# Performance work log

Hardware: AMD Instinct MI355X
Metric: run time of the kernel (lower is better)

## Reference

```python
import jax, jax.numpy as jnp
import numpy as np

NUM_GROUPS = 32
EPS = 1e-6


def group_norm(x, scale, bias):
    # x: [b, c, l]
    b, c, l = x.shape
    xg = x.reshape(b, NUM_GROUPS, (c // NUM_GROUPS) * l)
    mean = jnp.mean(xg, axis=2, keepdims=True)
    var = jnp.var(xg, axis=2, keepdims=True)
    xn = ((xg - mean) * jax.lax.rsqrt(var + EPS)).reshape(b, c, l)
    return xn * scale[None, :, None] + bias[None, :, None]


def conv1x1(x, w, b):
    # pointwise conv: w [out_c, in_c], x [b, in_c, l]
    return jnp.einsum('oc,bcl->bol', w, x) + b[None, :, None]


def setup_inputs() -> dict:
    key = jax.random.key(0)
    ks = jax.random.split(key, 11)
    b, c, l = 4, 512, 4096
    s = 1.0 / np.sqrt(c)
    return {
        'x': jax.random.normal(ks[0], (b, c, l), jnp.float32),
        'gn_scale': jnp.ones((c,), jnp.float32),
        'gn_bias': jnp.zeros((c,), jnp.float32),
        'wq': jax.random.normal(ks[1], (c, c), jnp.float32) * s,
        'bq': jnp.zeros((c,), jnp.float32),
        'wk': jax.random.normal(ks[2], (c, c), jnp.float32) * s,
        'bk': jnp.zeros((c,), jnp.float32),
        'wv': jax.random.normal(ks[3], (c, c), jnp.float32) * s,
        'bv': jnp.zeros((c,), jnp.float32),
        'wp': jax.random.normal(ks[4], (c, c), jnp.float32) * s,
        'bp': jnp.zeros((c,), jnp.float32),
    }


def reference(x, gn_scale, gn_bias, wq, bq, wk, bk, wv, bv, wp, bp):
    h_ = group_norm(x, gn_scale, gn_bias)
    q = conv1x1(h_, wq, bq)  # [b, c, l]
    k = conv1x1(h_, wk, bk)
    v = conv1x1(h_, wv, bv)
    c = q.shape[1]
    # scores w[b,i,j] = sum_c q[b,c,i] k[b,c,j] * c^-0.5, softmax over j
    w = jnp.einsum('bci,bcj->bij', q, k) * (c ** -0.5)
    w = jax.nn.softmax(w, axis=2)
    # out[b,c,i] = sum_j w[b,i,j] v[b,c,j]
    h_ = jnp.einsum('bij,bcj->bci', w, v)
    h_ = conv1x1(h_, wp, bp)
    return x + h_
```

## Files before the change

kernel.cpp:

```cpp
#include <hip/hip_runtime.h>
#include <math.h>

#define BB 4
#define CC 512
#define LL 4096
#define NG 32
#define CPG 16
#define EPSV 1e-6f

typedef short s16x8 __attribute__((ext_vector_type(8)));
typedef __bf16 bf8v __attribute__((ext_vector_type(8)));
typedef float f32x4 __attribute__((ext_vector_type(4)));
typedef float f32x16 __attribute__((ext_vector_type(16)));
typedef int i32x4 __attribute__((ext_vector_type(4)));
typedef int i32x8 __attribute__((ext_vector_type(8)));
typedef unsigned short u16;
typedef unsigned char u8;

typedef const __attribute__((address_space(1))) void g1_void;
typedef __attribute__((address_space(3))) void l3_void;

#define ASM_SBAR() asm volatile("s_barrier" ::: "memory")
#define ASM_WAITV(N) asm volatile("s_waitcnt vmcnt(" #N ")" ::: "memory")

static __device__ __forceinline__ float bf2f(u16 h) {
    unsigned int u = ((unsigned int)h) << 16;
    union { unsigned int u; float f; } c; c.u = u; return c.f;
}
static __device__ __forceinline__ u16 f2bf(float f) {
    union { float f; unsigned int u; } c; c.f = f;
    unsigned int lsb = (c.u >> 16) & 1u;
    c.u += 0x7fffu + lsb;
    return (u16)(c.u >> 16);
}
static __device__ __forceinline__ u8 f2fp8(float f) {
    int v = __builtin_amdgcn_cvt_pk_fp8_f32(f, f, 0, false);
    return (u8)(v & 0xff);
}
static __device__ __forceinline__ bf8v ld_bf8(const u16* p) {
    return *reinterpret_cast<const bf8v*>(p);
}
static __device__ __forceinline__ i32x8 ld32(const u8* plo, const u8* phi) {
    i32x4 lo = *reinterpret_cast<const i32x4*>(plo);
    i32x4 hi = *reinterpret_cast<const i32x4*>(phi);
    return __builtin_shufflevector(lo, hi, 0, 1, 2, 3, 4, 5, 6, 7);
}
#define MFMA_SC(a, b, c) \
    __builtin_amdgcn_mfma_scale_f32_32x32x64_f8f6f4(a, b, c, 0, 0, 0, 0x7f, 0, 0x7f)

static __device__ __forceinline__ void gload16(const u16* g, u16* l) {
    __builtin_amdgcn_global_load_lds((g1_void*)g, (l3_void*)l, 16, 0, 0);
}
static __device__ __forceinline__ void gload16b(const u8* g, u8* l) {
    __builtin_amdgcn_global_load_lds((g1_void*)g, (l3_void*)l, 16, 0, 0);
}

__global__ __launch_bounds__(256) void wconv_kernel(const float* __restrict__ w0,
                                                    const float* __restrict__ w1,
                                                    const float* __restrict__ w2,
                                                    const float* __restrict__ w3,
                                                    u16* __restrict__ wbf) {
    int i = blockIdx.x * 256 + threadIdx.x;
    int wsel = blockIdx.y;
    const float* src = (wsel == 0) ? w0 : (wsel == 1) ? w1 : (wsel == 2) ? w2 : w3;
    float4 v = reinterpret_cast<const float4*>(src)[i];
    ushort4 o;
    o.x = f2bf(v.x); o.y = f2bf(v.y); o.z = f2bf(v.z); o.w = f2bf(v.w);
    reinterpret_cast<ushort4*>(wbf + (size_t)wsel * CC * CC)[i] = o;
}

__global__ __launch_bounds__(256) void biascat_kernel(const float* __restrict__ bq,
                                                      const float* __restrict__ bk,
                                                      const float* __restrict__ bv,
                                                      float* __restrict__ bcat,
                                                      float* __restrict__ rowsum) {
    int i = blockIdx.x * 256 + threadIdx.x;
    if (i < 3 * CC) {
        float v = (i < CC) ? bq[i] : (i < 2 * CC ? bk[i - CC] : bv[i - 2 * CC]);
        bcat[i] = v;
    }
    if (i < BB * LL) rowsum[i] = 0.f;
}

__global__ __launch_bounds__(256) void gn_stats_kernel(const float* __restrict__ x,
                                                       float2* __restrict__ stats) {
    int g = blockIdx.x, b = blockIdx.y, t = threadIdx.x;
    const float4* xp = reinterpret_cast<const float4*>(x + ((size_t)b * CC + (size_t)g * CPG) * LL);
    float s = 0.f, ss = 0.f;
    for (int it = 0; it < 64; ++it) {
        float4 v = xp[it * 256 + t];
        s += v.x + v.y + v.z + v.w;
        ss += v.x * v.x + v.y * v.y + v.z * v.z + v.w * v.w;
    }
    #pragma unroll
    for (int off = 32; off; off >>= 1) { s += __shfl_xor(s, off, 64); ss += __shfl_xor(ss, off, 64); }
    __shared__ float rs[4], rss[4];
    int wave = t >> 6, lane = t & 63;
    if (lane == 0) { rs[wave] = s; rss[wave] = ss; }
    __syncthreads();
    if (t == 0) {
        float S = rs[0] + rs[1] + rs[2] + rs[3];
        float SS = rss[0] + rss[1] + rss[2] + rss[3];
        float mean = S * (1.f / 65536.f);
        float var = SS * (1.f / 65536.f) - mean * mean;
        var = fmaxf(var, 0.f);
        stats[b * NG + g] = make_float2(mean, rsqrtf(var + EPSV));
    }
}

__global__ __launch_bounds__(256) void gn_norm_t_kernel(const float* __restrict__ x,
                                                        const float2* __restrict__ stats,
                                                        const float* __restrict__ gsc,
                                                        const float* __restrict__ gbi,
                                                        u16* __restrict__ hT) {
    int lt = blockIdx.x, ct = blockIdx.y, b = blockIdx.z;
    __shared__ u16 tile[64][72];
    int t = threadIdx.x;
    int cl0 = t >> 4, c4 = (t & 15) * 4;
    #pragma unroll
    for (int p = 0; p < 4; ++p) {
        int cl = p * 16 + cl0;
        int cg = ct * 64 + cl;
        float2 st = stats[b * NG + (cg >> 4)];
        float sc = gsc[cg] * st.y;
        float bi = gbi[cg];
        float4 v = *reinterpret_cast<const float4*>(x + ((size_t)b * CC + cg) * LL + lt * 64 + c4);
        tile[cl][c4 + 0] = f2bf((v.x - st.x) * sc + bi);
        tile[cl][c4 + 1] = f2bf((v.y - st.x) * sc + bi);
        tile[cl][c4 + 2] = f2bf((v.z - st.x) * sc + bi);
        tile[cl][c4 + 3] = f2bf((v.w - st.x) * sc + bi);
    }
    __syncthreads();
    int r = t >> 3, c8 = (t & 7) * 8;
    #pragma unroll
    for (int p = 0; p < 2; ++p) {
        int ll = p * 32 + r;
        s16x8 ov;
        #pragma unroll
        for (int j = 0; j < 8; ++j) ov[j] = (short)tile[c8 + j][ll];
        u16* hp = hT + ((size_t)b * LL + lt * 64 + ll) * CC + ct * 64 + c8;
        *reinterpret_cast<s16x8*>(hp) = ov;
    }
}

template <int MODE>
__global__ __launch_bounds__(256) void gemm_kernel(const u16* __restrict__ A, size_t asb, int lda,
                                                   const u16* __restrict__ B, size_t bsb, int ldb,
                                                   const float* __restrict__ bias,
                                                   u8* __restrict__ Oq, u8* __restrict__ Ok,
                                                   u8* __restrict__ Ov, size_t osb,
                                                   const float* __restrict__ xres,
                                                   float* __restrict__ fout, int K) {
    __shared__ u16 pool[24576];
    u8* pool8 = (u8*)pool;
    int mt = blockIdx.x, nt = blockIdx.y, b = blockIdx.z;
    int t = threadIdx.x;
    int wave = t >> 6, lane = t & 63;
    int wm = (wave >> 1) * 64, wn = (wave & 1) * 64;
    int l15 = lane & 15, quad = lane >> 4;
    f32x4 acc[4][4] = {};
    const u16* Ab = A + (size_t)b * asb + (size_t)mt * 128 * lda;
    const u16* Bb = B + (size_t)b * bsb + (size_t)nt * 128 * ldb;
    int swzg = ((lane & 3) ^ ((lane >> 2) & 3) ^ ((lane >> 4) & 3)) * 8;
    int row0 = wave * 16 + (lane >> 2);
    int row1 = 64 + row0;
    const u16* Ap0 = Ab + (size_t)row0 * lda + swzg;
    const u16* Ap1 = Ab + (size_t)row1 * lda + swzg;
    const u16* Bp0 = Bb + (size_t)row0 * ldb + swzg;
    const u16* Bp1 = Bb + (size_t)row1 * ldb + swzg;
    int wo = wave * 512;
    int swzf = (l15 & 3) ^ (l15 >> 2);
    int aoff = (wm + l15) * 32 + ((quad ^ swzf) * 8);
    int boff = (wn + l15) * 32 + ((quad ^ swzf) * 8);
    const int iters = K >> 5;
    gload16(Ap0, pool + wo);                gload16(Ap1, pool + 2048 + wo);
    gload16(Bp0, pool + 12288 + wo);        gload16(Bp1, pool + 12288 + 2048 + wo);
    gload16(Ap0 + 32, pool + 4096 + wo);    gload16(Ap1 + 32, pool + 4096 + 2048 + wo);
    gload16(Bp0 + 32, pool + 16384 + wo);   gload16(Bp1 + 32, pool + 16384 + 2048 + wo);
    int bs = 0;
    for (int i = 0; i < iters; ++i) {
        if (i + 1 < iters) { ASM_WAITV(4); } else { ASM_WAITV(0); }
        ASM_SBAR();
        const u16* As = pool + bs;
        const u16* Bs = pool + 12288 + bs;
        bf8v af[4], bfr[4];
        #pragma unroll
        for (int ii = 0; ii < 4; ++ii)
            af[ii] = ld_bf8(&As[aoff + ii * 512]);
        #pragma unroll
        for (int j = 0; j < 4; ++j)
            bfr[j] = ld_bf8(&Bs[boff + j * 512]);
        if (i + 2 < iters) {
            int kk = (i + 2) * 32;
            int nb = bs + 8192; if (nb >= 12288) nb -= 12288;
            u16* as = pool + nb; u16* bsp = pool + 12288 + nb;
            gload16(Ap0 + kk, as + wo);        gload16(Ap1 + kk, as + 2048 + wo);
            gload16(Bp0 + kk, bsp + wo);       gload16(Bp1 + kk, bsp + 2048 + wo);
        }
        __builtin_amdgcn_s_setprio(1);
        #pragma unroll
        for (int ii = 0; ii < 4; ++ii)
            #pragma unroll
            for (int j = 0; j < 4; ++j)
                acc[ii][j] = __builtin_amdgcn_mfma_f32_16x16x32_bf16(af[ii], bfr[j], acc[ii][j], 0, 0, 0);
        __builtin_amdgcn_s_setprio(0);
        bs += 4096; if (bs >= 12288) bs -= 12288;
    }
    if (MODE == 0) {
        int nt_sel = nt >> 2, ntl = nt & 3;
        if (nt_sel == 2) {
            __syncthreads();
            #pragma unroll
            for (int j = 0; j < 4; ++j) {
                float bv = bias[nt * 128 + wn + j * 16 + l15];
                #pragma unroll
                for (int i = 0; i < 4; ++i) {
                    int col = wn + j * 16 + l15;
                    int row = wm + i * 16 + quad * 4;
                    unsigned int w = __builtin_amdgcn_cvt_pk_fp8_f32(acc[i][j][0] + bv, acc[i][j][1] + bv, 0, false);
                    w = __builtin_amdgcn_cvt_pk_fp8_f32(acc[i][j][2] + bv, acc[i][j][3] + bv, w, true);
                    *reinterpret_cast<unsigned int*>(&pool8[col * 144 + row]) = w;
                }
            }
            __syncthreads();
            u8* Ob = Ov + (size_t)b * osb + (size_t)(ntl * 128) * LL + mt * 128;
            #pragma unroll
            for (int it = 0; it < 4; ++it) {
                int idx = it * 256 + t;
                int row = idx >> 3, ch = (idx & 7) * 16;
                *reinterpret_cast<float4*>(Ob + (size_t)row * LL + ch) =
                    *reinterpret_cast<const float4*>(&pool8[row * 144 + ch]);
            }
        } else {
            u8* Oc = (nt_sel == 0 ? Oq : Ok) + (size_t)b * osb
                     + (size_t)(mt * 128) * CC + ntl * 128 + wn + l15;
            #pragma unroll
            for (int j = 0; j < 4; ++j) {
                float bv = bias[nt * 128 + wn + j * 16 + l15];
                #pragma unroll
                for (int i = 0; i < 4; ++i)
                    #pragma unroll
                    for (int r = 0; r < 4; ++r) {
                        int row = wm + i * 16 + quad * 4 + r;
                        Oc[(size_t)row * CC + j * 16] = f2fp8(acc[i][j][r] + bv);
                    }
            }
        }
    } else {
        __syncthreads();
        #pragma unroll
        for (int j = 0; j < 4; ++j) {
            float bv = bias[nt * 128 + wn + j * 16 + l15];
            #pragma unroll
            for (int i = 0; i < 4; ++i)
                #pragma unroll
                for (int r = 0; r < 4; ++r) {
                    int row = wm + i * 16 + quad * 4 + r;
                    int col = wn + j * 16 + l15;
                    pool[col * 136 + row] = f2bf(acc[i][j][r] + bv);
                }
        }
        __syncthreads();
        const float* xb = xres + ((size_t)b * CC + nt * 128) * LL + mt * 128;
        float* ob = fout + ((size_t)b * CC + nt * 128) * LL + mt * 128;
        #pragma unroll
        for (int it = 0; it < 16; ++it) {
            int idx = it * 256 + t;
            int cl = idx >> 5, ch = (idx & 31) * 4;
            short4 pv = *reinterpret_cast<const short4*>(&pool[cl * 136 + ch]);
            float4 xv = *reinterpret_cast<const float4*>(xb + (size_t)cl * LL + ch);
            float4 ov;
            ov.x = xv.x + bf2f((u16)pv.x);
            ov.y = xv.y + bf2f((u16)pv.y);
            ov.z = xv.z + bf2f((u16)pv.z);
            ov.w = xv.w + bf2f((u16)pv.w);
            *reinterpret_cast<float4*>(ob + (size_t)cl * LL + ch) = ov;
        }
    }
}

template <int MODE>
__global__ __launch_bounds__(256) void gemm8_kernel(const u8* __restrict__ A, size_t asb, int lda,
                                                    const u8* __restrict__ B, size_t bsb, int ldb,
                                                    float scale,
                                                    u8* __restrict__ Out8, u16* __restrict__ OutH,
                                                    size_t osb, int Nout, int K,
                                                    float* __restrict__ rsum) {
    __shared__ u8 pool8[MODE == 1 ? 32768 : 49152];
    int mt = blockIdx.x, nt = blockIdx.y, b = blockIdx.z;
    int t = threadIdx.x;
    int wave = t >> 6, lane = t & 63;
    int wm = (wave >> 1) * 64, wn = (wave & 1) * 64;
    int l15 = lane & 15, quad = lane >> 4;
    int l31 = lane & 31, hsel = lane >> 5;
    f32x4 acc16[4][4] = {};
    f32x16 accm[2][2] = {};
    int R = wave * 32 + (lane >> 1);
    int c16 = ((lane & 1) ^ (R & 1) ^ ((R >> 2) & 1)) * 16;
    const u8* Ap = A + (size_t)b * asb + (size_t)(mt * 128 + R) * lda + c16;
    const u8* Bp = B + (size_t)b * bsb + (size_t)(nt * 128 + R) * ldb + c16;
    int wo = wave * 1024;
    int p = (l15 & 1) ^ ((l15 >> 2) & 1);
    int fo = (((quad >> 1) ^ p) * 16) + (quad & 1) * 8;
    int abase = (wm + l15) * 32 + fo;
    int bbase = (wn + l15) * 32 + fo;
    int ra = wm + l31;
    int rb = wn + l31;
    int sa = (ra & 1) ^ ((ra >> 2) & 1);
    int sb = (rb & 1) ^ ((rb >> 2) & 1);
    int a_lo = hsel * 4096 + ra * 32 + sa * 16;
    int a_hi = hsel * 4096 + ra * 32 + 16 - sa * 16;
    int b_lo = hsel * 4096 + rb * 32 + sb * 16;
    int b_hi = hsel * 4096 + rb * 32 + 16 - sb * 16;
    if (MODE == 1) {
        const int iters = K >> 5;
        #define STG1(ii) do { size_t kk = (size_t)(ii) * 32; int bb = ((ii) & 3) * 4096; \
            gload16b(Ap + kk, pool8 + bb + wo);                                          \
            gload16b(Bp + kk, pool8 + 16384 + bb + wo); } while (0)
        STG1(0); STG1(1); STG1(2);
        for (int i = 0; i < iters; ++i) {
            if (i + 2 < iters) { ASM_WAITV(4); }
            else if (i + 1 < iters) { ASM_WAITV(2); }
            else { ASM_WAITV(0); }
            ASM_SBAR();
            int bb = (i & 3) * 4096;
            const u8* As = pool8 + bb;
            const u8* Bs = pool8 + 16384 + bb;
            long af[4], bf[4];
            #pragma unroll
            for (int ii = 0; ii < 4; ++ii)
                af[ii] = *reinterpret_cast<const long*>(As + abase + ii * 512);
            #pragma unroll
            for (int j = 0; j < 4; ++j)
                bf[j] = *reinterpret_cast<const long*>(Bs + bbase + j * 512);
            if (i + 3 < iters) STG1(i + 3);
            __builtin_amdgcn_s_setprio(1);
            #pragma unroll
            for (int ii = 0; ii < 4; ++ii)
                #pragma unroll
                for (int j = 0; j < 4; ++j)
                    acc16[ii][j] = __builtin_amdgcn_mfma_f32_16x16x32_fp8_fp8(af[ii], bf[j], acc16[ii][j], 0, 0, 0);
            __builtin_amdgcn_s_setprio(0);
        }
        #undef STG1
        u8* Ob = Out8 + (size_t)b * osb + (size_t)(mt * 128) * Nout + nt * 128 + wn + l15;
        #pragma unroll
        for (int i = 0; i < 4; ++i) {
            #pragma unroll
            for (int r = 0; r < 4; ++r) {
                int row = wm + i * 16 + quad * 4 + r;
                u8* rp = Ob + (size_t)row * Nout;
                float part = 0.f;
                #pragma unroll
                for (int j = 0; j < 4; ++j) {
                    float v = __expf(acc16[i][j][r] * scale - 3.0f);
                    part += v;
                    rp[j * 16] = f2fp8(v);
                }
                part += __shfl_xor(part, 1, 64);
                part += __shfl_xor(part, 2, 64);
                part += __shfl_xor(part, 4, 64);
                part += __shfl_xor(part, 8, 64);
                if (l15 == 0)
                    atomicAdd(rsum + (size_t)b * LL + mt * 128 + row, part);
            }
        }
    } else {
        const int iters = K >> 6;
        #define STG2(ii, bsv) do { size_t kk = (size_t)(ii) * 64;              \
            gload16b(Ap + kk,      pool8 + (bsv) + wo);                        \
            gload16b(Ap + kk + 32, pool8 + (bsv) + 4096 + wo);                 \
            gload16b(Bp + kk,      pool8 + 24576 + (bsv) + wo);                \
            gload16b(Bp + kk + 32, pool8 + 24576 + (bsv) + 4096 + wo); } while (0)
        STG2(0, 0);
        STG2(1, 8192);
        int bs = 0;
        for (int i = 0; i < iters; ++i) {
            if (i + 1 < iters) { ASM_WAITV(4); } else { ASM_WAITV(0); }
            ASM_SBAR();
            const u8* As = pool8 + bs;
            const u8* Bs = pool8 + 24576 + bs;
            i32x8 a0 = ld32(As + a_lo, As + a_hi);
            i32x8 a1 = ld32(As + 1024 + a_lo, As + 1024 + a_hi);
            i32x8 b0 = ld32(Bs + b_lo, Bs + b_hi);
            i32x8 b1 = ld32(Bs + 1024 + b_lo, Bs + 1024 + b_hi);
            if (i + 2 < iters) {
                int nb = bs + 16384; if (nb >= 24576) nb -= 24576;
                STG2(i + 2, nb);
            }
            __builtin_amdgcn_s_setprio(1);
            accm[0][0] = MFMA_SC(a0, b0, accm[0][0]);
            accm[0][1] = MFMA_SC(a0, b1, accm[0][1]);
            accm[1][0] = MFMA_SC(a1, b0, accm[1][0]);
            accm[1][1] = MFMA_SC(a1, b1, accm[1][1]);
            __builtin_amdgcn_s_setprio(0);
            bs += 8192; if (bs >= 24576) bs -= 24576;
        }
        #undef STG2
        __syncthreads();
        u16* poolh = (u16*)pool8;
        const float* rbase2 = rsum + (size_t)b * LL + mt * 128;
        #pragma unroll
        for (int i = 0; i < 2; ++i)
            #pragma unroll
            for (int rg = 0; rg < 4; ++rg) {
                int row0 = wm + i * 32 + 8 * rg + 4 * hsel;
                float4 rv = *reinterpret_cast<const float4*>(rbase2 + row0);
                float iv[4] = {1.f / rv.x, 1.f / rv.y, 1.f / rv.z, 1.f / rv.w};
                #pragma unroll
                for (int rr = 0; rr < 4; ++rr) {
                    int reg = rg * 4 + rr;
                    int row = row0 + rr;
                    poolh[row * 136 + wn + l31]      = f2bf(accm[i][0][reg] * iv[rr]);
                    poolh[row * 136 + wn + 32 + l31] = f2bf(accm[i][1][reg] * iv[rr]);
                }
            }
        __syncthreads();
        u16* Ob = OutH + (size_t)b * osb + (size_t)(mt * 128) * Nout + nt * 128;
        #pragma unroll
        for (int it = 0; it < 8; ++it) {
            int idx = it * 256 + t;
            int row = idx >> 4, ch = (idx & 15) * 8;
            s16x8 val = *reinterpret_cast<const s16x8*>(&poolh[row * 136 + ch]);
            *reinterpret_cast<s16x8*>(Ob + (size_t)row * Nout + ch) = val;
        }
    }
}

extern "C" void kernel_launch(void* const* d_in, const int* in_sizes, int n_in,
                              void* d_out, int out_size, void* d_ws, size_t ws_size,
                              hipStream_t stream) {
    const float* x   = (const float*)d_in[0];
    const float* gsc = (const float*)d_in[1];
    const float* gbi = (const float*)d_in[2];
    const float* wq  = (const float*)d_in[3];
    const float* bq  = (const float*)d_in[4];
    const float* wk  = (const float*)d_in[5];
    const float* bk  = (const float*)d_in[6];
    const float* wv  = (const float*)d_in[7];
    const float* bv  = (const float*)d_in[8];
    const float* wp  = (const float*)d_in[9];
    const float* bp  = (const float*)d_in[10];
    float* out = (float*)d_out;

    char* ws = (char*)d_ws;
    const size_t SZ   = (size_t)BB * LL * CC * 2;
    const size_t QSZ  = (size_t)BB * LL * CC;
    const size_t WQSZ = (size_t)4 * CC * CC * 2;
    const size_t RSZ  = (size_t)BB * LL * 4;
    u16* bufA = (u16*)(ws);
    u8*  q8   = (u8*)(ws + SZ);
    u8*  k8   = (u8*)(ws + SZ + QSZ);
    u8*  v8   = (u8*)(ws + SZ + 2 * QSZ);
    u16* wbf  = (u16*)(ws + SZ + 3 * QSZ);
    float2* stats = (float2*)(ws + SZ + 3 * QSZ + WQSZ);
    float* bcat   = (float*)(ws + SZ + 3 * QSZ + WQSZ + 4096);
    float* rowsum = (float*)(ws + SZ + 3 * QSZ + WQSZ + 4096 + 8192);
    u8* S8 = (u8*)(ws + SZ + 3 * QSZ + WQSZ + 4096 + 8192 + RSZ);
    const float scale = 0.044194173824159216f;
    const size_t BLC = (size_t)LL * CC;

    wconv_kernel<<<dim3(256, 4), 256, 0, stream>>>(wq, wk, wv, wp, wbf);
    biascat_kernel<<<dim3(64), 256, 0, stream>>>(bq, bk, bv, bcat, rowsum);
    gn_stats_kernel<<<dim3(NG, BB), 256, 0, stream>>>(x, stats);
    gn_norm_t_kernel<<<dim3(64, 8, BB), 256, 0, stream>>>(x, stats, gsc, gbi, bufA);
    gemm_kernel<0><<<dim3(32, 12, BB), 256, 0, stream>>>(bufA, BLC, CC, wbf, 0, CC, bcat,
                                                         q8, k8, v8, BLC, nullptr, nullptr, CC);
    gemm8_kernel<1><<<dim3(32, 32, BB), 256, 0, stream>>>(q8, BLC, CC, k8, BLC, CC, scale,
                                                          S8, nullptr, (size_t)LL * LL, LL, CC, rowsum);
    gemm8_kernel<2><<<dim3(32, 4, BB), 256, 0, stream>>>(S8, (size_t)LL * LL, LL, v8, BLC, LL, 1.f,
                                                         nullptr, bufA, BLC, CC, LL, rowsum);
    gemm_kernel<3><<<dim3(32, 4, BB), 256, 0, stream>>>(bufA, BLC, CC, wbf + 3 * CC * CC, 0, CC,
                                                        bp, nullptr, nullptr, nullptr, 0, x, out, CC);
}
```

Baseline: 311.6 us.

## Replace QK^T score GEMM with single-wave 64x64 tile kernel without barriers

The score GEMM (Q·K^T with exp and row-sum) moves out of the templated 4-wave 128x128 kernel into a dedicated single-wave kernel that computes 64x64 tiles, launching 64x64x4 blocks. With one wave per block, the LDS pipeline (triple buffered, 12KB) needs no s_barrier, and each block stays small so more blocks can be resident per CU. The cost is less operand reuse per block: each wave loads both A and B tiles itself, which doubles global/L2 traffic for Q and K relative to 128x128 tiles. The PV GEMM kernel is de-templated with no functional change.

```diff
diff --git a/kernel.cpp b/kernel.cpp
--- a/kernel.cpp
+++ b/kernel.cpp
@@ -279,31 +279,100 @@
     }
 }
 
-template <int MODE>
+__global__ __launch_bounds__(64) void gemm8s_kernel(const u8* __restrict__ A,
+                                                    const u8* __restrict__ B,
+                                                    float scale,
+                                                    u8* __restrict__ Out8,
+                                                    float* __restrict__ rsum) {
+    __shared__ u8 pool8[12288];
+    int mt = blockIdx.x, nt = blockIdx.y, b = blockIdx.z;
+    int lane = threadIdx.x;
+    int l15 = lane & 15, quad = lane >> 4;
+    f32x4 acc[4][4] = {};
+    int R = lane >> 1;
+    int c16 = ((lane & 1) ^ (R & 1) ^ ((R >> 2) & 1)) * 16;
+    const size_t BLC = (size_t)LL * CC;
+    const u8* Ap = A + (size_t)b * BLC + (size_t)(mt * 64 + R) * CC + c16;
+    const u8* Bp = B + (size_t)b * BLC + (size_t)(nt * 64 + R) * CC + c16;
+    int p = (l15 & 1) ^ ((l15 >> 2) & 1);
+    int fo = (((quad >> 1) ^ p) * 16) + (quad & 1) * 8;
+    int abase = l15 * 32 + fo;
+    #define STGS(ii, bb) do { size_t kk = (size_t)(ii) * 32;               \
+        gload16b(Ap + kk,           pool8 + (bb));                         \
+        gload16b(Ap + 32 * CC + kk, pool8 + (bb) + 1024);                  \
+        gload16b(Bp + kk,           pool8 + (bb) + 2048);                  \
+        gload16b(Bp + 32 * CC + kk, pool8 + (bb) + 3072); } while (0)
+    const int iters = CC >> 5;
+    STGS(0, 0);
+    STGS(1, 4096);
+    int bs = 0;
+    for (int i = 0; i < iters; ++i) {
+        if (i + 1 < iters) { ASM_WAITV(4); } else { ASM_WAITV(0); }
+        const u8* As = pool8 + bs;
+        const u8* Bs = pool8 + bs + 2048;
+        long af[4], bf[4];
+        #pragma unroll
+        for (int ii = 0; ii < 4; ++ii)
+            af[ii] = *reinterpret_cast<const long*>(As + abase + ii * 512);
+        #pragma unroll
+        for (int j = 0; j < 4; ++j)
+            bf[j] = *reinterpret_cast<const long*>(Bs + abase + j * 512);
+        if (i + 2 < iters) {
+            int nb = bs + 8192; if (nb >= 12288) nb -= 12288;
+            STGS(i + 2, nb);
+        }
+        __builtin_amdgcn_s_setprio(1);
+        #pragma unroll
+        for (int ii = 0; ii < 4; ++ii)
+            #pragma unroll
+            for (int j = 0; j < 4; ++j)
+                acc[ii][j] = __builtin_amdgcn_mfma_f32_16x16x32_fp8_fp8(af[ii], bf[j], acc[ii][j], 0, 0, 0);
+        __builtin_amdgcn_s_setprio(0);
+        bs += 4096; if (bs >= 12288) bs -= 12288;
+    }
+    #undef STGS
+    u8* Ob = Out8 + (size_t)b * ((size_t)LL * LL) + (size_t)(mt * 64) * LL + nt * 64 + l15;
+    float* rbase = rsum + (size_t)b * LL + mt * 64;
+    #pragma unroll
+    for (int i = 0; i < 4; ++i) {
+        #pragma unroll
+        for (int r = 0; r < 4; ++r) {
+            int row = i * 16 + quad * 4 + r;
+            u8* rp = Ob + (size_t)row * LL;
+            float part = 0.f;
+            #pragma unroll
+            for (int j = 0; j < 4; ++j) {
+                float v = __expf(acc[i][j][r] * scale - 3.0f);
+                part += v;
+                rp[j * 16] = f2fp8(v);
+            }
+            part += __shfl_xor(part, 1, 64);
+            part += __shfl_xor(part, 2, 64);
+            part += __shfl_xor(part, 4, 64);
+            part += __shfl_xor(part, 8, 64);
+            if (l15 == 0)
+                atomicAdd(rbase + row, part);
+        }
+    }
+}
+
 __global__ __launch_bounds__(256) void gemm8_kernel(const u8* __restrict__ A, size_t asb, int lda,
                                                     const u8* __restrict__ B, size_t bsb, int ldb,
-                                                    float scale,
-                                                    u8* __restrict__ Out8, u16* __restrict__ OutH,
+                                                    u16* __restrict__ OutH,
                                                     size_t osb, int Nout, int K,
-                                                    float* __restrict__ rsum) {
-    __shared__ u8 pool8[MODE == 1 ? 32768 : 49152];
+                                                    const float* __restrict__ rsum) {
+    __shared__ u8 pool8[49152];
     int mt = blockIdx.x, nt = blockIdx.y, b = blockIdx.z;
     int t = threadIdx.x;
     int wave = t >> 6, lane = t & 63;
     int wm = (wave >> 1) * 64, wn = (wave & 1) * 64;
-    int l15 = lane & 15, quad = lane >> 4;
     int l31 = lane & 31, hsel = lane >> 5;
-    f32x4 acc16[4][4] = {};
     f32x16 accm[2][2] = {};
     int R = wave * 32 + (lane >> 1);
     int c16 = ((lane & 1) ^ (R & 1) ^ ((R >> 2) & 1)) * 16;
     const u8* Ap = A + (size_t)b * asb + (size_t)(mt * 128 + R) * lda + c16;
     const u8* Bp = B + (size_t)b * bsb + (size_t)(nt * 128 + R) * ldb + c16;
     int wo = wave * 1024;
-    int p = (l15 & 1) ^ ((l15 >> 2) & 1);
-    int fo = (((quad >> 1) ^ p) * 16) + (quad & 1) * 8;
-    int abase = (wm + l15) * 32 + fo;
-    int bbase = (wn + l15) * 32 + fo;
     int ra = wm + l31;
     int rb = wn + l31;
     int sa = (ra & 1) ^ ((ra >> 2) & 1);
@@ -312,118 +381,63 @@
     int a_hi = hsel * 4096 + ra * 32 + 16 - sa * 16;
     int b_lo = hsel * 4096 + rb * 32 + sb * 16;
     int b_hi = hsel * 4096 + rb * 32 + 16 - sb * 16;
-    if (MODE == 1) {
-        const int iters = K >> 5;
-        #define STG1(ii) do { size_t kk = (size_t)(ii) * 32; int bb = ((ii) & 3) * 4096; \
-            gload16b(Ap + kk, pool8 + bb + wo);                                          \
-            gload16b(Bp + kk, pool8 + 16384 + bb + wo); } while (0)
-        STG1(0); STG1(1); STG1(2);
-        for (int i = 0; i < iters; ++i) {
-            if (i + 2 < iters) { ASM_WAITV(4); }
-            else if (i + 1 < iters) { ASM_WAITV(2); }
-            else { ASM_WAITV(0); }
-            ASM_SBAR();
-            int bb = (i & 3) * 4096;
-            const u8* As = pool8 + bb;
-            const u8* Bs = pool8 + 16384 + bb;
-            long af[4], bf[4];
-            #pragma unroll
-            for (int ii = 0; ii < 4; ++ii)
-                af[ii] = *reinterpret_cast<const long*>(As + abase + ii * 512);
-            #pragma unroll
-            for (int j = 0; j < 4; ++j)
-                bf[j] = *reinterpret_cast<const long*>(Bs + bbase + j * 512);
-            if (i + 3 < iters) STG1(i + 3);
-            __builtin_amdgcn_s_setprio(1);
-            #pragma unroll
-            for (int ii = 0; ii < 4; ++ii)
-                #pragma unroll
-                for (int j = 0; j < 4; ++j)
-                    acc16[ii][j] = __builtin_amdgcn_mfma_f32_16x16x32_fp8_fp8(af[ii], bf[j], acc16[ii][j], 0, 0, 0);
-            __builtin_amdgcn_s_setprio(0);
-        }
-        #undef STG1
-        u8* Ob = Out8 + (size_t)b * osb + (size_t)(mt * 128) * Nout + nt * 128 + wn + l15;
-        #pragma unroll
-        for (int i = 0; i < 4; ++i) {
-            #pragma unroll
-            for (int r = 0; r < 4; ++r) {
-                int row = wm + i * 16 + quad * 4 + r;
-                u8* rp = Ob + (size_t)row * Nout;
-                float part = 0.f;
-                #pragma unroll
-                for (int j = 0; j < 4; ++j) {
-                    float v = __expf(acc16[i][j][r] * scale - 3.0f);
-                    part += v;
-                    rp[j * 16] = f2fp8(v);
-                }
-                part += __shfl_xor(part, 1, 64);
-                part += __shfl_xor(part, 2, 64);
-                part += __shfl_xor(part, 4, 64);
-                part += __shfl_xor(part, 8, 64);
-                if (l15 == 0)
-                    atomicAdd(rsum + (size_t)b * LL + mt * 128 + row, part);
+    const int iters = K >> 6;
+    #define STG2(ii, bsv) do { size_t kk = (size_t)(ii) * 64;              \
+        gload16b(Ap + kk,      pool8 + (bsv) + wo);                        \
+        gload16b(Ap + kk + 32, pool8 + (bsv) + 4096 + wo);                 \
+        gload16b(Bp + kk,      pool8 + 24576 + (bsv) + wo);                \
+        gload16b(Bp + kk + 32, pool8 + 24576 + (bsv) + 4096 + wo); } while (0)
+    STG2(0, 0);
+    STG2(1, 8192);
+    int bs = 0;
+    for (int i = 0; i < iters; ++i) {
+        if (i + 1 < iters) { ASM_WAITV(4); } else { ASM_WAITV(0); }
+        ASM_SBAR();
+        const u8* As = pool8 + bs;
+        const u8* Bs = pool8 + 24576 + bs;
+        i32x8 a0 = ld32(As + a_lo, As + a_hi);
+        i32x8 a1 = ld32(As + 1024 + a_lo, As + 1024 + a_hi);
+        i32x8 b0 = ld32(Bs + b_lo, Bs + b_hi);
+        i32x8 b1 = ld32(Bs + 1024 + b_lo, Bs + 1024 + b_hi);
+        if (i + 2 < iters) {
+            int nb = bs + 16384; if (nb >= 24576) nb -= 24576;
+            STG2(i + 2, nb);
+        }
+        __builtin_amdgcn_s_setprio(1);
+        accm[0][0] = MFMA_SC(a0, b0, accm[0][0]);
+        accm[0][1] = MFMA_SC(a0, b1, accm[0][1]);
+        accm[1][0] = MFMA_SC(a1, b0, accm[1][0]);
+        accm[1][1] = MFMA_SC(a1, b1, accm[1][1]);
+        __builtin_amdgcn_s_setprio(0);
+        bs += 8192; if (bs >= 24576) bs -= 24576;
+    }
+    #undef STG2
+    __syncthreads();
+    u16* poolh = (u16*)pool8;
+    const float* rbase2 = rsum + (size_t)b * LL + mt * 128;
+    #pragma unroll
+    for (int i = 0; i < 2; ++i)
+        #pragma unroll
+        for (int rg = 0; rg < 4; ++rg) {
+            int row0 = wm + i * 32 + 8 * rg + 4 * hsel;
+            float4 rv = *reinterpret_cast<const float4*>(rbase2 + row0);
+            float iv[4] = {1.f / rv.x, 1.f / rv.y, 1.f / rv.z, 1.f / rv.w};
+            #pragma unroll
+            for (int rr = 0; rr < 4; ++rr) {
+                int reg = rg * 4 + rr;
+                int row = row0 + rr;
+                poolh[row * 136 + wn + l31]      = f2bf(accm[i][0][reg] * iv[rr]);
+                poolh[row * 136 + wn + 32 + l31] = f2bf(accm[i][1][reg] * iv[rr]);
             }
         }
-    } else {
-        const int iters = K >> 6;
-        #define STG2(ii, bsv) do { size_t kk = (size_t)(ii) * 64;              \
-            gload16b(Ap + kk,      pool8 + (bsv) + wo);                        \
-            gload16b(Ap + kk + 32, pool8 + (bsv) + 4096 + wo);                 \
-            gload16b(Bp + kk,      pool8 + 24576 + (bsv) + wo);                \
-            gload16b(Bp + kk + 32, pool8 + 24576 + (bsv) + 4096 + wo); } while (0)
-        STG2(0, 0);
-        STG2(1, 8192);
-        int bs = 0;
-        for (int i = 0; i < iters; ++i) {
-            if (i + 1 < iters) { ASM_WAITV(4); } else { ASM_WAITV(0); }
-            ASM_SBAR();
-            const u8* As = pool8 + bs;
-            const u8* Bs = pool8 + 24576 + bs;
-            i32x8 a0 = ld32(As + a_lo, As + a_hi);
-            i32x8 a1 = ld32(As + 1024 + a_lo, As + 1024 + a_hi);
-            i32x8 b0 = ld32(Bs + b_lo, Bs + b_hi);
-            i32x8 b1 = ld32(Bs + 1024 + b_lo, Bs + 1024 + b_hi);
-            if (i + 2 < iters) {
-                int nb = bs + 16384; if (nb >= 24576) nb -= 24576;
-                STG2(i + 2, nb);
-            }
-            __builtin_amdgcn_s_setprio(1);
-            accm[0][0] = MFMA_SC(a0, b0, accm[0][0]);
-            accm[0][1] = MFMA_SC(a0, b1, accm[0][1]);
-            accm[1][0] = MFMA_SC(a1, b0, accm[1][0]);
-            accm[1][1] = MFMA_SC(a1, b1, accm[1][1]);
-            __builtin_amdgcn_s_setprio(0);
-            bs += 8192; if (bs >= 24576) bs -= 24576;
-        }
-        #undef STG2
-        __syncthreads();
-        u16* poolh = (u16*)pool8;
-        const float* rbase2 = rsum + (size_t)b * LL + mt * 128;
-        #pragma unroll
-        for (int i = 0; i < 2; ++i)
-            #pragma unroll
-            for (int rg = 0; rg < 4; ++rg) {
-                int row0 = wm + i * 32 + 8 * rg + 4 * hsel;
-                float4 rv = *reinterpret_cast<const float4*>(rbase2 + row0);
-                float iv[4] = {1.f / rv.x, 1.f / rv.y, 1.f / rv.z, 1.f / rv.w};
-                #pragma unroll
-                for (int rr = 0; rr < 4; ++rr) {
-                    int reg = rg * 4 + rr;
-                    int row = row0 + rr;
-                    poolh[row * 136 + wn + l31]      = f2bf(accm[i][0][reg] * iv[rr]);
-                    poolh[row * 136 + wn + 32 + l31] = f2bf(accm[i][1][reg] * iv[rr]);
-                }
-            }
-        __syncthreads();
-        u16* Ob = OutH + (size_t)b * osb + (size_t)(mt * 128) * Nout + nt * 128;
-        #pragma unroll
-        for (int it = 0; it < 8; ++it) {
-            int idx = it * 256 + t;
-            int row = idx >> 4, ch = (idx & 15) * 8;
-            s16x8 val = *reinterpret_cast<const s16x8*>(&poolh[row * 136 + ch]);
-            *reinterpret_cast<s16x8*>(Ob + (size_t)row * Nout + ch) = val;
-        }
+    __syncthreads();
+    u16* Ob = OutH + (size_t)b * osb + (size_t)(mt * 128) * Nout + nt * 128;
+    #pragma unroll
+    for (int it = 0; it < 8; ++it) {
+        int idx = it * 256 + t;
+        int row = idx >> 4, ch = (idx & 15) * 8;
+        s16x8 val = *reinterpret_cast<const s16x8*>(&poolh[row * 136 + ch]);
+        *reinterpret_cast<s16x8*>(Ob + (size_t)row * Nout + ch) = val;
     }
 }
 
@@ -466,10 +480,9 @@
     gn_norm_t_kernel<<<dim3(64, 8, BB), 256, 0, stream>>>(x, stats, gsc, gbi, bufA);
     gemm_kernel<0><<<dim3(32, 12, BB), 256, 0, stream>>>(bufA, BLC, CC, wbf, 0, CC, bcat,
                                                          q8, k8, v8, BLC, nullptr, nullptr, CC);
-    gemm8_kernel<1><<<dim3(32, 32, BB), 256, 0, stream>>>(q8, BLC, CC, k8, BLC, CC, scale,
-                                                          S8, nullptr, (size_t)LL * LL, LL, CC, rowsum);
-    gemm8_kernel<2><<<dim3(32, 4, BB), 256, 0, stream>>>(S8, (size_t)LL * LL, LL, v8, BLC, LL, 1.f,
-                                                         nullptr, bufA, BLC, CC, LL, rowsum);
+    gemm8s_kernel<<<dim3(64, 64, BB), 64, 0, stream>>>(q8, k8, scale, S8, rowsum);
+    gemm8_kernel<<<dim3(32, 4, BB), 256, 0, stream>>>(S8, (size_t)LL * LL, LL, v8, BLC, LL,
+                                                      bufA, BLC, CC, LL, rowsum);
     gemm_kernel<3><<<dim3(32, 4, BB), 256, 0, stream>>>(bufA, BLC, CC, wbf + 3 * CC * CC, 0, CC,
                                                         bp, nullptr, nullptr, nullptr, 0, x, out, CC);
 }
```

Measured after the change: 355.0 us. 13.9% more time.
